# Kernel optimization log

Measured on AMD Instinct MI355X. Metric: run time of the kernel, lower is better.

The kernel has to match this reference:

```python
import jax, jax.numpy as jnp
import numpy as np

B, L, HID = 2, 2048, 2048
H = 16
QL = 1536      # q_lora_rank
KVL = 512      # kv_lora_rank
ROPE = 64      # qk_rope_head_dim
NOPE = 128     # qk_nope_head_dim
VD = 128       # v_head_dim
QKD = NOPE + ROPE
SCALE = QKD ** -0.5
EPS = 1e-5
THETA = 10000.0
SQ = (HID / QL) ** 0.5    # mla_scale_q_lora
SKV = (HID / KVL) ** 0.5  # mla_scale_kv_lora


def rmsnorm(x, w, eps=EPS):
    return x * jax.lax.rsqrt(jnp.mean(x * x, axis=-1, keepdims=True) + eps) * w


def rope_traditional(x, base=THETA):
    # x: [..., L, D]; traditional (interleaved-pair) RoPE, offset 0
    D = x.shape[-1]
    Lx = x.shape[-2]
    freqs = base ** (-jnp.arange(0, D, 2, dtype=jnp.float32) / D)  # [D/2]
    th = jnp.arange(Lx, dtype=jnp.float32)[:, None] * freqs[None, :]  # [L, D/2]
    cos, sin = jnp.cos(th), jnp.sin(th)
    x1, x2 = x[..., 0::2], x[..., 1::2]
    r1 = x1 * cos - x2 * sin
    r2 = x1 * sin + x2 * cos
    return jnp.stack([r1, r2], axis=-1).reshape(x.shape)


def setup_inputs() -> dict:
    key = jax.random.key(0)
    ks = jax.random.split(key, 9)
    s = 0.02
    x = jax.random.normal(ks[0], (B, L, HID), dtype=jnp.float32)
    mask = jnp.tril(jnp.ones((L, L), dtype=bool))[None, None]  # causal [1,1,L,L]
    wq_a = jax.random.normal(ks[1], (QL, HID), dtype=jnp.float32) * s
    q_a_ln_w = jnp.ones((QL,), dtype=jnp.float32)
    wq_b = jax.random.normal(ks[2], (H * QKD, QL), dtype=jnp.float32) * s
    wkv_a = jax.random.normal(ks[3], (KVL + ROPE, HID), dtype=jnp.float32) * s
    kv_a_ln_w = jnp.ones((KVL,), dtype=jnp.float32)
    w_embed_q = jax.random.normal(ks[4], (H, KVL, NOPE), dtype=jnp.float32) * s  # [H,out,in]
    w_unembed = jax.random.normal(ks[5], (H, VD, KVL), dtype=jnp.float32) * s    # [H,out,in]
    wo = jax.random.normal(ks[6], (HID, H * VD), dtype=jnp.float32) * s
    return {"x": x, "mask": mask, "wq_a": wq_a, "q_a_ln_w": q_a_ln_w,
            "wq_b": wq_b, "wkv_a": wkv_a, "kv_a_ln_w": kv_a_ln_w,
            "w_embed_q": w_embed_q, "w_unembed": w_unembed, "wo": wo}


def reference(x, mask, wq_a, q_a_ln_w, wq_b, wkv_a, kv_a_ln_w, w_embed_q, w_unembed, wo):
    b, l, _ = x.shape
    # q LoRA path: q_b(RMSNorm(q_a(x)))
    q = rmsnorm(x @ wq_a.T, q_a_ln_w) @ wq_b.T                # [b,l,H*QKD]
    q = q.reshape(b, l, H, QKD).transpose(0, 2, 1, 3) * SQ    # [b,H,l,QKD]
    q_nope, q_pe = q[..., :NOPE], q[..., NOPE:]
    # compressed kv + shared rope key
    ckv = x @ wkv_a.T                                         # [b,l,KVL+ROPE]
    kv_latent = rmsnorm(ckv[..., :KVL], kv_a_ln_w) * SKV      # [b,l,KVL]
    k_pe = ckv[..., KVL:]                                     # [b,l,ROPE] (single shared head)
    q_pe = rope_traditional(q_pe)
    k_pe = rope_traditional(k_pe)
    # rope scores as additive bias, with boolean mask baked in
    pe = jnp.einsum('bhqd,bkd->bhqk', q_pe * SCALE, k_pe)     # [b,H,l,l]
    pe = jnp.where(mask, pe, jnp.finfo(pe.dtype).min)
    # prefill path: up-project latent per head
    k = jnp.einsum('blk,hkn->bhln', kv_latent, w_embed_q)     # transpose=False: x @ W -> [b,H,l,NOPE]
    v = jnp.einsum('blk,hvk->bhlv', kv_latent, w_unembed)     # x @ W^T -> [b,H,l,VD]
    scores = jnp.einsum('bhqd,bhkd->bhqk', q_nope, k) * SCALE + pe
    attn = jax.nn.softmax(scores, axis=-1)
    out = jnp.einsum('bhqk,bhkv->bhqv', attn, v)              # [b,H,l,VD]
    out = out.transpose(0, 2, 1, 3).reshape(b, l, H * VD)
    return out @ wo.T
```

## Files before the change

kernel.cpp:

```cpp
#include <hip/hip_runtime.h>
#include <hip/hip_bf16.h>

#define B_SZ   2
#define L_SEQ  2048
#define HIDD   2048
#define NH     16
#define QL     1536
#define KVLR   512
#define ROPE_D 64
#define NOPE_D 128
#define VD     128
#define QKD    192

typedef __attribute__((ext_vector_type(8))) __bf16 bf16x8;
typedef __attribute__((ext_vector_type(4))) float  f32x4;
typedef __attribute__((ext_vector_type(8))) unsigned short u16x8;

#if __has_builtin(__builtin_amdgcn_exp2f)
#define EXP2(x) __builtin_amdgcn_exp2f(x)
#else
#define EXP2(x) exp2f(x)
#endif

__device__ __forceinline__ float bf2f(unsigned short u) {
    union { float f; unsigned int i; } x; x.i = ((unsigned int)u) << 16; return x.f;
}
__device__ __forceinline__ unsigned short f2bf(float f) {
    __hip_bfloat16 h = __float2bfloat16(f);
    return *reinterpret_cast<unsigned short*>(&h);
}
__device__ __forceinline__ float finclamp(float v) {
    return fminf(fmaxf(v, -3.3e38f), 3.3e38f);
}

__device__ __forceinline__ void gld_lds16(const __hip_bfloat16* g, __hip_bfloat16* l)
{
    __builtin_amdgcn_global_load_lds(
        (const __attribute__((address_space(1))) unsigned int*)(g),
        (__attribute__((address_space(3))) unsigned int*)(l),
        16, 0, 0);
}

__global__ void detect_fp32(const unsigned short* __restrict__ x, int* __restrict__ flag)
{
    if (threadIdx.x == 0 && blockIdx.x == 0) {
        int c = 0;
        for (int i = 0; i < 128; i++) {
            unsigned e = (x[2 * i] >> 7) & 0xFF;
            if (e > 150 || (e > 0 && e < 100)) c++;
        }
        *flag = (c >= 16) ? 1 : 0;
    }
}

struct ConvDesc {
    const void* src[9];
    __hip_bfloat16* dst[9];
    long long n8[9];
};

__global__ __launch_bounds__(256)
void conv_all(ConvDesc d, const int* __restrict__ flag)
{
    const int seg = blockIdx.y;
    const void* src = d.src[seg];
    __hip_bfloat16* dst = d.dst[seg];
    const long long n8 = d.n8[seg];
    const int isf = *flag;
    long long stride = (long long)gridDim.x * 256;
    for (long long i = (long long)blockIdx.x * 256 + threadIdx.x; i < n8; i += stride) {
        u16x8 o;
        if (isf) {
            const float* s = (const float*)src + i * 8;
            float4 a = *(const float4*)s;
            float4 b = *(const float4*)(s + 4);
            o[0] = f2bf(a.x); o[1] = f2bf(a.y); o[2] = f2bf(a.z); o[3] = f2bf(a.w);
            o[4] = f2bf(b.x); o[5] = f2bf(b.y); o[6] = f2bf(b.z); o[7] = f2bf(b.w);
        } else {
            o = ((const u16x8*)src)[i];
        }
        ((u16x8*)dst)[i] = o;
    }
}

__global__ __launch_bounds__(256)
void gemm_bt(const __hip_bfloat16* __restrict__ A,
             const __hip_bfloat16* __restrict__ Bm,
             void* __restrict__ Cv,
             int M, int N, int K, int lda, int ldb, int ldc,
             float scale,
             int dA, int mA, long long sA,
             int dB, int mB, long long sB, long long sC,
             const int* __restrict__ flagp, int fp32out)
{
    int z = blockIdx.z;
    A  += (long long)((z / dA) % mA) * sA;
    Bm += (long long)((z / dB) % mB) * sB;
    const long long coff = (long long)z * sC;

    __shared__ __hip_bfloat16 As[128 * 32];
    __shared__ __hip_bfloat16 Bs[128 * 32];

    const int tid  = threadIdx.x;
    const int lane = tid & 63;
    const int wid  = tid >> 6;
    const int quad = lane >> 4;
    const int l15  = lane & 15;
    const int wm   = (wid >> 1) * 64;
    const int wn   = (wid & 1) * 64;

    const int m0 = blockIdx.y * 128;
    const int n0 = blockIdx.x * 128;

    const int srow = lane >> 2;
    const int scol = (lane & 3) * 8;

    f32x4 acc[4][4] = {};

    for (int k0 = 0; k0 < K; k0 += 32) {
        __syncthreads();
        for (int i = 0; i < 2; i++) {
            int rbase = wid * 32 + i * 16;
            int r = rbase + srow;
            gld_lds16(A + (long long)(m0 + r) * lda + k0 + scol, &As[rbase * 32]);
            int gn = n0 + r; if (gn >= N) gn = N - 1;
            gld_lds16(Bm + (long long)gn * ldb + k0 + scol, &Bs[rbase * 32]);
        }
        __syncthreads();

        bf16x8 af[4], bfv[4];
        for (int mt = 0; mt < 4; mt++)
            af[mt] = *reinterpret_cast<const bf16x8*>(
                &As[(wm + mt * 16 + l15) * 32 + quad * 8]);
        for (int nt = 0; nt < 4; nt++)
            bfv[nt] = *reinterpret_cast<const bf16x8*>(
                &Bs[(wn + nt * 16 + l15) * 32 + quad * 8]);
        for (int mt = 0; mt < 4; mt++)
            for (int nt = 0; nt < 4; nt++)
                acc[mt][nt] = __builtin_amdgcn_mfma_f32_16x16x32_bf16(
                    af[mt], bfv[nt], acc[mt][nt], 0, 0, 0);
    }

    const int f32o = fp32out && (*flagp);

    for (int mt = 0; mt < 4; mt++) {
        int row = m0 + wm + mt * 16 + quad * 4;
        for (int nt = 0; nt < 4; nt++) {
            int col = n0 + wn + nt * 16 + l15;
            if (col < N) {
                for (int r = 0; r < 4; r++) {
                    float val = finclamp(acc[mt][nt][r] * scale);
                    long long idx = coff + (long long)(row + r) * ldc + col;
                    if (f32o) ((float*)Cv)[idx] = val;
                    else      ((__hip_bfloat16*)Cv)[idx] = __float2bfloat16(val);
                }
            }
        }
    }
}

__global__ __launch_bounds__(256)
void rope_q(__hip_bfloat16* __restrict__ Q)
{
    int row = blockIdx.x;
    int l = row & (L_SEQ - 1);
    int tid = threadIdx.x;
    for (int p = tid; p < NH * 32; p += 256) {
        int h = p >> 5, i = p & 31;
        __hip_bfloat16* base = Q + (long long)row * (NH * QKD) + h * QKD + NOPE_D + 2 * i;
        float freq = exp2f(-(float)i * (13.287712379549449f / 32.0f));
        float th = (float)l * freq;
        float s = __sinf(th), c = __cosf(th);
        float x1 = __bfloat162float(base[0]);
        float x2 = __bfloat162float(base[1]);
        base[0] = __float2bfloat16(finclamp(x1 * c - x2 * s));
        base[1] = __float2bfloat16(finclamp(x1 * s + x2 * c));
    }
}

__global__ __launch_bounds__(256)
void rmsnorm_qa(__hip_bfloat16* __restrict__ X, const __hip_bfloat16* __restrict__ W,
                int ldx)
{
    int row = blockIdx.x;
    __hip_bfloat16* xr = X + (long long)row * ldx;
    int tid = threadIdx.x;
    bool act = tid < (QL / 8);
    float v[8];
    float ss = 0.f;
    if (act) {
        u16x8 raw = *reinterpret_cast<const u16x8*>(xr + tid * 8);
        for (int j = 0; j < 8; j++) {
            v[j] = bf2f(((const unsigned short*)&raw)[j]);
            ss += v[j] * v[j];
        }
    }
    for (int m = 1; m < 64; m <<= 1) ss += __shfl_xor(ss, m, 64);
    __shared__ float ws4[4];
    if ((tid & 63) == 0) ws4[tid >> 6] = ss;
    __syncthreads();
    float tot = ws4[0] + ws4[1] + ws4[2] + ws4[3];
    float inv = rsqrtf(tot / (float)QL + 1e-5f);
    if (act) {
        u16x8 wr = *reinterpret_cast<const u16x8*>(W + tid * 8);
        u16x8 o;
        for (int j = 0; j < 8; j++)
            ((unsigned short*)&o)[j] =
                f2bf(finclamp(v[j] * inv * bf2f(((const unsigned short*)&wr)[j])));
        *reinterpret_cast<u16x8*>(xr + tid * 8) = o;
    }
}

__global__ __launch_bounds__(256)
void kv_norm_rope(const __hip_bfloat16* __restrict__ CQ,
                  const __hip_bfloat16* __restrict__ W,
                  __hip_bfloat16* __restrict__ KVLAT,
                  __hip_bfloat16* __restrict__ KPE)
{
    int row = blockIdx.x * 4 + (threadIdx.x >> 6);
    int l = row & (L_SEQ - 1);
    int t = threadIdx.x & 63;
    const __hip_bfloat16* cr = CQ + (long long)row * 2112;

    float v[8]; float ss = 0.f;
    u16x8 raw = *reinterpret_cast<const u16x8*>(cr + t * 8);
    for (int j = 0; j < 8; j++) {
        v[j] = bf2f(((const unsigned short*)&raw)[j]);
        ss += v[j] * v[j];
    }
    for (int m = 1; m < 64; m <<= 1) ss += __shfl_xor(ss, m, 64);
    float inv = rsqrtf(ss / (float)KVLR + 1e-5f) * 2.0f;
    u16x8 wr = *reinterpret_cast<const u16x8*>(W + t * 8);
    u16x8 o;
    for (int j = 0; j < 8; j++)
        ((unsigned short*)&o)[j] =
            f2bf(finclamp(v[j] * inv * bf2f(((const unsigned short*)&wr)[j])));
    *reinterpret_cast<u16x8*>(KVLAT + (long long)row * KVLR + t * 8) = o;

    if (t < 32) {
        float freq = exp2f(-(float)t * (13.287712379549449f / 32.0f));
        float th = (float)l * freq;
        float s = __sinf(th), c = __cosf(th);
        float x1 = __bfloat162float(cr[512 + 2 * t]);
        float x2 = __bfloat162float(cr[512 + 2 * t + 1]);
        __hip_bfloat16* kp = KPE + (long long)row * 64;
        kp[2 * t]     = __float2bfloat16(finclamp(x1 * c - x2 * s));
        kp[2 * t + 1] = __float2bfloat16(finclamp(x1 * s + x2 * c));
    }
}

__global__ __launch_bounds__(256)
void transpose_embed(const __hip_bfloat16* __restrict__ WE,
                     __hip_bfloat16* __restrict__ WB)
{
    int h = blockIdx.y;
    int k0 = blockIdx.x * 64;
    __shared__ __hip_bfloat16 t[64][136];
    int tid = threadIdx.x;
    for (int it = 0; it < 4; it++) {
        int s = tid + it * 256;
        int k = s >> 4, cg = (s & 15) * 8;
        u16x8 v = *reinterpret_cast<const u16x8*>(
            WE + ((long long)h * KVLR + k0 + k) * NOPE_D + cg);
        *reinterpret_cast<u16x8*>(&t[k][cg]) = v;
    }
    __syncthreads();
    for (int it = 0; it < 4; it++) {
        int s = tid + it * 256;
        int n = s >> 3, kg = (s & 7) * 8;
        u16x8 o;
        for (int j = 0; j < 8; j++)
            ((unsigned short*)&o)[j] = *reinterpret_cast<unsigned short*>(&t[kg + j][n]);
        *reinterpret_cast<u16x8*>(WB + ((long long)h * 128 + n) * KVLR + k0 + kg) = o;
    }
}

__global__ __launch_bounds__(256)
void flash_attn(const __hip_bfloat16* __restrict__ Q,
                const __hip_bfloat16* __restrict__ Kb,
                const __hip_bfloat16* __restrict__ Vt,
                const __hip_bfloat16* __restrict__ KPE,
                float* __restrict__ O0, float* __restrict__ O1,
                float* __restrict__ L0, float* __restrict__ L1)
{
    const int u = blockIdx.x;
    int qt, ch;
    if (u < 32) { int k = u >> 1; qt = 31 - k; ch = u & 1; }
    else        { qt = 47 - u;    ch = 0; }
    const int q0 = qt * 64;
    const int t0 = ch ? 16 : 0;
    const int t1 = ch ? (qt + 1) : ((qt + 1 < 16) ? (qt + 1) : 16);

    const int bh = blockIdx.y;
    const int b = bh >> 4;
    const int h = bh & 15;

    __shared__ __hip_bfloat16 Ks[64 * 200];
    __shared__ __hip_bfloat16 Vs[128 * 72];
    __shared__ __hip_bfloat16 Ps[4][16 * 72];

    const int tid  = threadIdx.x;
    const int lane = tid & 63;
    const int w    = tid >> 6;
    const int quad = lane >> 4;
    const int l15  = lane & 15;

    const __hip_bfloat16* Kbh  = Kb + (long long)bh * L_SEQ * 128;
    const __hip_bfloat16* Vth  = Vt + (long long)bh * 128 * L_SEQ;
    const __hip_bfloat16* KPEb = KPE + (long long)b * L_SEQ * 64;

    bf16x8 qf[6];
    {
        long long qoff = (long long)(b * L_SEQ + q0 + w * 16 + l15) * (NH * QKD) + h * QKD;
        for (int kk = 0; kk < 6; kk++)
            qf[kk] = *reinterpret_cast<const bf16x8*>(Q + qoff + kk * 32 + quad * 8);
    }

    f32x4 o_acc[8] = {};
    float l_run[4] = {0.f, 0.f, 0.f, 0.f};

    for (int kt = t0; kt < t1; kt++) {
        const int kk0 = kt * 64;
        const bool partial = (kt == qt);
        __syncthreads();
        for (int it = 0; it < 6; it++) {
            int s = tid + it * 256;
            int r = s / 24, cg = s % 24;
            u16x8 v;
            if (cg < 16)
                v = *reinterpret_cast<const u16x8*>(
                    Kbh + (long long)(kk0 + r) * 128 + cg * 8);
            else
                v = *reinterpret_cast<const u16x8*>(
                    KPEb + (long long)(kk0 + r) * 64 + (cg - 16) * 8);
            *reinterpret_cast<u16x8*>(&Ks[r * 200 + cg * 8]) = v;
        }
        for (int it = 0; it < 4; it++) {
            int s = tid + it * 256;
            int vd = s >> 3, kg = (s & 7) * 8;
            u16x8 v = *reinterpret_cast<const u16x8*>(
                Vth + (long long)vd * L_SEQ + kk0 + kg);
            *reinterpret_cast<u16x8*>(&Vs[vd * 72 + kg]) = v;
        }
        __syncthreads();

        f32x4 sfr[4];
        for (int nt = 0; nt < 4; nt++) {
            f32x4 sacc = {};
            for (int kk = 0; kk < 6; kk++) {
                bf16x8 kf = *reinterpret_cast<const bf16x8*>(
                    &Ks[(nt * 16 + l15) * 200 + kk * 32 + quad * 8]);
                sacc = __builtin_amdgcn_mfma_f32_16x16x32_bf16(qf[kk], kf, sacc, 0, 0, 0);
            }
            sfr[nt] = sacc;
        }

        const int qrow_base = q0 + w * 16 + quad * 4;
        float rs[4] = {0.f, 0.f, 0.f, 0.f};
        if (partial) {
            for (int nt = 0; nt < 4; nt++) {
                int key = kk0 + nt * 16 + l15;
                for (int r = 0; r < 4; r++) {
                    float p = (key > qrow_base + r) ? 0.f : EXP2(sfr[nt][r]);
                    sfr[nt][r] = p;
                    rs[r] += p;
                }
            }
        } else {
            for (int nt = 0; nt < 4; nt++)
                for (int r = 0; r < 4; r++) {
                    float p = EXP2(sfr[nt][r]);
                    sfr[nt][r] = p;
                    rs[r] += p;
                }
        }

        for (int nt = 0; nt < 4; nt++)
            for (int r = 0; r < 4; r++)
                Ps[w][(quad * 4 + r) * 72 + nt * 16 + l15] =
                    __float2bfloat16(sfr[nt][r]);

        for (int r = 0; r < 4; r++) {
            float t = rs[r];
            for (int m = 1; m < 16; m <<= 1) t += __shfl_xor(t, m, 16);
            l_run[r] += t;
        }

        for (int ks = 0; ks < 2; ks++) {
            bf16x8 pf = *reinterpret_cast<const bf16x8*>(
                &Ps[w][l15 * 72 + ks * 32 + quad * 8]);
            for (int vt = 0; vt < 8; vt++) {
                bf16x8 vf = *reinterpret_cast<const bf16x8*>(
                    &Vs[(vt * 16 + l15) * 72 + ks * 32 + quad * 8]);
                o_acc[vt] = __builtin_amdgcn_mfma_f32_16x16x32_bf16(pf, vf, o_acc[vt], 0, 0, 0);
            }
        }
    }

    const int orow = q0 + w * 16 + quad * 4;
    float* Op; float* Lp; long long rbase;
    if (ch == 0) { Op = O0; Lp = L0; rbase = (long long)b * 2048 + orow; }
    else         { Op = O1; Lp = L1; rbase = (long long)b * 1024 + (orow - 1024); }
    for (int r = 0; r < 4; r++) {
        float* op = Op + (rbase + r) * 2048 + h * 128;
        for (int vt = 0; vt < 8; vt++)
            op[vt * 16 + l15] = o_acc[vt][r];
        if (l15 == 0) Lp[(rbase + r) * 16 + h] = l_run[r];
    }
}

__global__ __launch_bounds__(256)
void combine_o(const float* __restrict__ O0, const float* __restrict__ O1,
               const float* __restrict__ L0, const float* __restrict__ L1,
               __hip_bfloat16* __restrict__ aout)
{
    const int row = blockIdx.x;
    const int rl = row & 2047;
    const int b = row >> 11;
    const bool has1 = rl >= 1024;
    const long long rowc = (long long)b * 1024 + (rl - 1024);
    const float* o0 = O0 + (long long)row * 2048;
    const float* o1 = O1 + rowc * 2048;
    const int tid = threadIdx.x;
    const int c0 = tid * 8;
    const int h = c0 >> 7;
    float l = L0[(long long)row * 16 + h] + (has1 ? L1[rowc * 16 + h] : 0.f);
    float inv = 1.0f / fmaxf(l, 1e-30f);
    float4 a = *(const float4*)(o0 + c0);
    float4 bb = *(const float4*)(o0 + c0 + 4);
    if (has1) {
        float4 c = *(const float4*)(o1 + c0);
        float4 d = *(const float4*)(o1 + c0 + 4);
        a.x += c.x; a.y += c.y; a.z += c.z; a.w += c.w;
        bb.x += d.x; bb.y += d.y; bb.z += d.z; bb.w += d.w;
    }
    u16x8 o;
    o[0] = f2bf(finclamp(a.x * inv));  o[1] = f2bf(finclamp(a.y * inv));
    o[2] = f2bf(finclamp(a.z * inv));  o[3] = f2bf(finclamp(a.w * inv));
    o[4] = f2bf(finclamp(bb.x * inv)); o[5] = f2bf(finclamp(bb.y * inv));
    o[6] = f2bf(finclamp(bb.z * inv)); o[7] = f2bf(finclamp(bb.w * inv));
    *reinterpret_cast<u16x8*>(aout + (long long)row * 2048 + c0) = o;
}

extern "C" void kernel_launch(void* const* d_in, const int* in_sizes, int n_in,
                              void* d_out, int out_size, void* d_ws, size_t ws_size,
                              hipStream_t stream)
{
    const long long want[9] = {
        8388608, 3145728, 1536, 4718592, 1179648, 512, 1048576, 1048576, 4194304
    };
    const void* P[9] = {};
    {
        int j = 0;
        for (int i = 0; i < n_in && j < 9; i++)
            if ((long long)in_sizes[i] == want[j]) P[j++] = d_in[i];
        if (!P[8]) {
            const int map[9] = {0, 2, 3, 4, 5, 6, 7, 8, 9};
            for (int j2 = 0; j2 < 9; j2++) P[j2] = d_in[map[j2]];
        }
    }
    (void)ws_size; (void)out_size;

    char* ws = (char*)d_ws;
    int* flag = (int*)ws;
    char* A = ws + 256;

    __hip_bfloat16* xc     = (__hip_bfloat16*)(A);
    __hip_bfloat16* wfused = (__hip_bfloat16*)(A + 16777216);
    __hip_bfloat16* wqbc   = (__hip_bfloat16*)(A + 25427968);
    __hip_bfloat16* cq     = (__hip_bfloat16*)(A + 34865152);
    float* O0 = (float*)(A);
    float* O1 = (float*)(A + 33554432);
    float* L0 = (float*)(A + 50331648);
    float* L1 = (float*)(A + 50593792);

    long long off = 256 + 52166656;
    auto alloc = [&](long long bytes) {
        char* p = ws + off;
        off += ((bytes + 255) / 256) * 256;
        return p;
    };
    __hip_bfloat16* qlnwc  = (__hip_bfloat16*)alloc(3072);
    __hip_bfloat16* kvlnwc = (__hip_bfloat16*)alloc(1024);
    __hip_bfloat16* wembc  = (__hip_bfloat16*)alloc(2097152);
    __hip_bfloat16* wunec  = (__hip_bfloat16*)alloc(2097152);
    __hip_bfloat16* woc    = (__hip_bfloat16*)alloc(8388608);
    __hip_bfloat16* kvl    = (__hip_bfloat16*)alloc(4194304);
    __hip_bfloat16* kpe    = (__hip_bfloat16*)alloc(524288);
    __hip_bfloat16* wBk    = (__hip_bfloat16*)alloc(2097152);
    __hip_bfloat16* kvK    = (__hip_bfloat16*)alloc(16777216);
    __hip_bfloat16* kvVt   = (__hip_bfloat16*)alloc(16777216);
    __hip_bfloat16* qbuf   = (__hip_bfloat16*)alloc(25165824);
    __hip_bfloat16* aout   = (__hip_bfloat16*)alloc(16777216);

    detect_fp32<<<1, 64, 0, stream>>>((const unsigned short*)P[0], flag);
    ConvDesc cd;
    cd.src[0] = P[0]; cd.dst[0] = xc;                  cd.n8[0] = 8388608 / 8;
    cd.src[1] = P[4]; cd.dst[1] = wfused;              cd.n8[1] = 1179648 / 8;
    cd.src[2] = P[1]; cd.dst[2] = wfused + 576LL*2048; cd.n8[2] = 3145728 / 8;
    cd.src[3] = P[2]; cd.dst[3] = qlnwc;               cd.n8[3] = 1536 / 8;
    cd.src[4] = P[3]; cd.dst[4] = wqbc;                cd.n8[4] = 4718592 / 8;
    cd.src[5] = P[5]; cd.dst[5] = kvlnwc;              cd.n8[5] = 512 / 8;
    cd.src[6] = P[6]; cd.dst[6] = wembc;               cd.n8[6] = 1048576 / 8;
    cd.src[7] = P[7]; cd.dst[7] = wunec;               cd.n8[7] = 1048576 / 8;
    cd.src[8] = P[8]; cd.dst[8] = woc;                 cd.n8[8] = 4194304 / 8;
    conv_all<<<dim3(512, 9), 256, 0, stream>>>(cd, flag);

    gemm_bt<<<dim3(17, 32, 1), 256, 0, stream>>>(
        xc, wfused, cq, 4096, 2112, 2048, 2048, 2048, 2112, 1.0f,
        1, 1, 0, 1, 1, 0, 0, flag, 0);
    kv_norm_rope<<<1024, 256, 0, stream>>>(cq, kvlnwc, kvl, kpe);
    transpose_embed<<<dim3(8, 16), 256, 0, stream>>>(wembc, wBk);
    gemm_bt<<<dim3(1, 16, 32), 256, 0, stream>>>(
        kvl, wBk, kvK, 2048, 128, 512, 512, 512, 128, 1.0f,
        16, 2, (long long)L_SEQ * KVLR, 1, 16, 128LL * KVLR,
        (long long)L_SEQ * 128, flag, 0);
    gemm_bt<<<dim3(16, 1, 32), 256, 0, stream>>>(
        wunec, kvl, kvVt, 128, 2048, 512, 512, 512, 2048, 1.0f,
        1, 16, 128LL * KVLR, 16, 2, (long long)L_SEQ * KVLR,
        128LL * L_SEQ, flag, 0);
    rmsnorm_qa<<<4096, 256, 0, stream>>>(cq + 576, qlnwc, 2112);
    gemm_bt<<<dim3(24, 32, 1), 256, 0, stream>>>(
        cq + 576, wqbc, qbuf, 4096, 3072, 1536, 2112, 1536, 3072,
        0.1202245867417521f,
        1, 1, 0, 1, 1, 0, 0, flag, 0);
    rope_q<<<4096, 256, 0, stream>>>(qbuf);
    flash_attn<<<dim3(48, 32), 256, 0, stream>>>(
        qbuf, kvK, kvVt, kpe, O0, O1, L0, L1);
    combine_o<<<4096, 256, 0, stream>>>(O0, O1, L0, L1, aout);
    gemm_bt<<<dim3(16, 32, 1), 256, 0, stream>>>(
        aout, woc, (void*)d_out, 4096, 2048, 2048, 2048, 2048, 2048, 1.0f,
        1, 1, 0, 1, 1, 0, 0, flag, 1);
}
```

Measured before the change: 537.0 us.

## Split attention KV range into four chunks and store bf16 partials

The flash attention grid now splits each query tile's key range into up to four chunks of 512 keys, giving 80 blocks per head instead of 48. This balances the causal workload better and raises parallelism. Partial outputs are stored as bf16 instead of fp32 to cut write and read traffic, and the combine kernel sums up to four partials. The trade-offs are more partial-buffer traffic from the extra chunks and some precision loss from rounding the unnormalized partials to bf16. It appears to rely on a fixed, non-running-max softmax so partials add directly.

New measurement: 530.7 us. No clear change (-1.2%).

```diff
diff --git a/kernel.cpp b/kernel.cpp
--- a/kernel.cpp
+++ b/kernel.cpp
@@ -280,16 +280,18 @@
                 const __hip_bfloat16* __restrict__ Kb,
                 const __hip_bfloat16* __restrict__ Vt,
                 const __hip_bfloat16* __restrict__ KPE,
-                float* __restrict__ O0, float* __restrict__ O1,
-                float* __restrict__ L0, float* __restrict__ L1)
+                __hip_bfloat16* __restrict__ OP,
+                float* __restrict__ LP)
 {
     const int u = blockIdx.x;
-    int qt, ch;
-    if (u < 32) { int k = u >> 1; qt = 31 - k; ch = u & 1; }
-    else        { qt = 47 - u;    ch = 0; }
+    int c, qt;
+    if (u < 32)      { c = 0; qt = 31 - u; }
+    else if (u < 56) { c = 1; qt = 31 - (u - 32); }
+    else if (u < 72) { c = 2; qt = 31 - (u - 56); }
+    else             { c = 3; qt = 31 - (u - 72); }
     const int q0 = qt * 64;
-    const int t0 = ch ? 16 : 0;
-    const int t1 = ch ? (qt + 1) : ((qt + 1 < 16) ? (qt + 1) : 16);
+    const int t0 = c * 8;
+    const int t1 = (qt + 1 < t0 + 8) ? (qt + 1) : (t0 + 8);
 
     const int bh = blockIdx.y;
     const int b = bh >> 4;
@@ -397,48 +399,43 @@
         }
     }
 
+    const int pfx[4] = {0, 4096, 7168, 9216};
     const int orow = q0 + w * 16 + quad * 4;
-    float* Op; float* Lp; long long rbase;
-    if (ch == 0) { Op = O0; Lp = L0; rbase = (long long)b * 2048 + orow; }
-    else         { Op = O1; Lp = L1; rbase = (long long)b * 1024 + (orow - 1024); }
+    const long long rb0 = pfx[c] + (long long)b * (2048 - 512 * c) + (orow - 512 * c);
     for (int r = 0; r < 4; r++) {
-        float* op = Op + (rbase + r) * 2048 + h * 128;
+        __hip_bfloat16* op = OP + (rb0 + r) * 2048 + h * 128;
         for (int vt = 0; vt < 8; vt++)
-            op[vt * 16 + l15] = o_acc[vt][r];
-        if (l15 == 0) Lp[(rbase + r) * 16 + h] = l_run[r];
-    }
-}
-
-__global__ __launch_bounds__(256)
-void combine_o(const float* __restrict__ O0, const float* __restrict__ O1,
-               const float* __restrict__ L0, const float* __restrict__ L1,
+            op[vt * 16 + l15] = __float2bfloat16(finclamp(o_acc[vt][r]));
+        if (l15 == 0) LP[(rb0 + r) * 16 + h] = l_run[r];
+    }
+}
+
+__global__ __launch_bounds__(256)
+void combine_o(const __hip_bfloat16* __restrict__ OP, const float* __restrict__ LP,
                __hip_bfloat16* __restrict__ aout)
 {
     const int row = blockIdx.x;
     const int rl = row & 2047;
     const int b = row >> 11;
-    const bool has1 = rl >= 1024;
-    const long long rowc = (long long)b * 1024 + (rl - 1024);
-    const float* o0 = O0 + (long long)row * 2048;
-    const float* o1 = O1 + rowc * 2048;
+    const int nch = (rl >> 9) + 1;
     const int tid = threadIdx.x;
     const int c0 = tid * 8;
     const int h = c0 >> 7;
-    float l = L0[(long long)row * 16 + h] + (has1 ? L1[rowc * 16 + h] : 0.f);
+    const int pfx[4] = {0, 4096, 7168, 9216};
+
+    float acc[8] = {};
+    float l = 0.f;
+    for (int c = 0; c < nch; c++) {
+        long long rb = pfx[c] + (long long)b * (2048 - 512 * c) + (rl - 512 * c);
+        l += LP[rb * 16 + h];
+        u16x8 v = *reinterpret_cast<const u16x8*>(OP + rb * 2048 + c0);
+        for (int j = 0; j < 8; j++)
+            acc[j] += bf2f(((const unsigned short*)&v)[j]);
+    }
     float inv = 1.0f / fmaxf(l, 1e-30f);
-    float4 a = *(const float4*)(o0 + c0);
-    float4 bb = *(const float4*)(o0 + c0 + 4);
-    if (has1) {
-        float4 c = *(const float4*)(o1 + c0);
-        float4 d = *(const float4*)(o1 + c0 + 4);
-        a.x += c.x; a.y += c.y; a.z += c.z; a.w += c.w;
-        bb.x += d.x; bb.y += d.y; bb.z += d.z; bb.w += d.w;
-    }
     u16x8 o;
-    o[0] = f2bf(finclamp(a.x * inv));  o[1] = f2bf(finclamp(a.y * inv));
-    o[2] = f2bf(finclamp(a.z * inv));  o[3] = f2bf(finclamp(a.w * inv));
-    o[4] = f2bf(finclamp(bb.x * inv)); o[5] = f2bf(finclamp(bb.y * inv));
-    o[6] = f2bf(finclamp(bb.z * inv)); o[7] = f2bf(finclamp(bb.w * inv));
+    for (int j = 0; j < 8; j++)
+        ((unsigned short*)&o)[j] = f2bf(finclamp(acc[j] * inv));
     *reinterpret_cast<u16x8*>(aout + (long long)row * 2048 + c0) = o;
 }
 
@@ -469,10 +466,8 @@
     __hip_bfloat16* wfused = (__hip_bfloat16*)(A + 16777216);
     __hip_bfloat16* wqbc   = (__hip_bfloat16*)(A + 25427968);
     __hip_bfloat16* cq     = (__hip_bfloat16*)(A + 34865152);
-    float* O0 = (float*)(A);
-    float* O1 = (float*)(A + 33554432);
-    float* L0 = (float*)(A + 50331648);
-    float* L1 = (float*)(A + 50593792);
+    __hip_bfloat16* OP = (__hip_bfloat16*)(A);
+    float*          LP = (float*)(A + 41943040);
 
     long long off = 256 + 52166656;
     auto alloc = [&](long long bytes) {
@@ -525,9 +520,9 @@
         0.1202245867417521f,
         1, 1, 0, 1, 1, 0, 0, flag, 0);
     rope_q<<<4096, 256, 0, stream>>>(qbuf);
-    flash_attn<<<dim3(48, 32), 256, 0, stream>>>(
-        qbuf, kvK, kvVt, kpe, O0, O1, L0, L1);
-    combine_o<<<4096, 256, 0, stream>>>(O0, O1, L0, L1, aout);
+    flash_attn<<<dim3(80, 32), 256, 0, stream>>>(
+        qbuf, kvK, kvVt, kpe, OP, LP);
+    combine_o<<<4096, 256, 0, stream>>>(OP, LP, aout);
     gemm_bt<<<dim3(16, 32, 1), 256, 0, stream>>>(
         aout, woc, (void*)d_out, 4096, 2048, 2048, 2048, 2048, 2048, 1.0f,
         1, 1, 0, 1, 1, 0, 0, flag, 1);
```
